# Optimization experiments

Measured on AMD Instinct MI355X. Metric: run time of the kernel, lower is better.

## Reference

```python
import jax, jax.numpy as jnp
import numpy as np

C = 1024
D = C // 8  # query/key channel dim


def setup_inputs() -> dict:
    key = jax.random.key(0)
    ks = jax.random.split(key, 8)
    x = jax.random.normal(ks[0], (8, C, 2048), dtype=jnp.float32)
    # 1x1 Conv1d == per-position linear over channels: weight [out, in], bias [out]
    s_qk = 1.0 / np.sqrt(C)
    Wq = jax.random.uniform(ks[1], (D, C), jnp.float32, -s_qk, s_qk)
    bq = jax.random.uniform(ks[2], (D,), jnp.float32, -s_qk, s_qk)
    Wk = jax.random.uniform(ks[3], (D, C), jnp.float32, -s_qk, s_qk)
    bk = jax.random.uniform(ks[4], (D,), jnp.float32, -s_qk, s_qk)
    Wv = jax.random.uniform(ks[5], (C, C), jnp.float32, -s_qk, s_qk)
    bv = jax.random.uniform(ks[6], (C,), jnp.float32, -s_qk, s_qk)
    gamma = jnp.zeros((1,), dtype=jnp.float32)
    return {"x": x, "Wq": Wq, "bq": bq, "Wk": Wk, "bk": bk, "Wv": Wv, "bv": bv, "gamma": gamma}


def reference(x, Wq, bq, Wk, bk, Wv, bv, gamma):
    # x: [b, c, l]
    q = jnp.einsum('dc,bcl->bdl', Wq, x) + bq[None, :, None]  # [b, d, l]
    k = jnp.einsum('dc,bcl->bdl', Wk, x) + bk[None, :, None]  # [b, d, l]
    v = jnp.einsum('oc,bcl->bol', Wv, x) + bv[None, :, None]  # [b, c, l]
    energy = jnp.einsum('bdi,bdj->bij', q, k)                  # [b, l, l] (no scale, as in source)
    attention = jax.nn.softmax(energy, axis=-1)
    out = jnp.einsum('bcj,bij->bci', v, attention)             # value @ attention^T
    return gamma * out + x
```

## Files before the change

### kernel.cpp

```cpp
#include <hip/hip_runtime.h>
#include <hip/hip_bf16.h>
#include <stdint.h>

#define B_ 8
#define C_ 1024
#define D_ 128
#define L_ 2048

typedef __attribute__((ext_vector_type(8))) short short8;
typedef __attribute__((ext_vector_type(4))) float floatx4;

#define GLDS16(g, l)                                                          \
    __builtin_amdgcn_global_load_lds(                                         \
        (const __attribute__((address_space(1))) uint32_t*)(g),               \
        (__attribute__((address_space(3))) uint32_t*)(l), 16, 0, 0)

__device__ inline float b2f(uint16_t u) {
    union { uint32_t i; float f; } x; x.i = (uint32_t)u << 16; return x.f;
}
__device__ inline uint16_t f2b(float f) {
    union { uint32_t i; float f; } x; x.f = f;
    uint32_t r = (x.i + 0x7fff + ((x.i >> 16) & 1)) >> 16;
    return (uint16_t)r;
}

__global__ void cast_f32_bf16(const float* __restrict__ src, uint16_t* __restrict__ dst, int n) {
    int i = blockIdx.x * 256 + threadIdx.x;
    if (i < n) dst[i] = f2b(src[i]);
}

__global__ __launch_bounds__(256) void transpose_cast(const float* __restrict__ x, uint16_t* __restrict__ xT) {
    __shared__ float tile[32][33];
    int b = blockIdx.z;
    int l0 = blockIdx.x * 32, c0 = blockIdx.y * 32;
    int tx = threadIdx.x, ty = threadIdx.y;
    const float* xb = x + (size_t)b * C_ * L_;
#pragma unroll
    for (int i = 0; i < 4; i++)
        tile[ty + i * 8][tx] = xb[(size_t)(c0 + ty + i * 8) * L_ + l0 + tx];
    __syncthreads();
    uint16_t* xtb = xT + (size_t)b * L_ * C_;
#pragma unroll
    for (int i = 0; i < 4; i++) {
        int l = l0 + ty + i * 8, c = c0 + tx;
        xtb[(size_t)l * C_ + c] = f2b(tile[tx][ty + i * 8]);
    }
}

__global__ __launch_bounds__(256) void gemm_qk(
    const uint16_t* __restrict__ A, const uint16_t* __restrict__ B, long sB,
    const float* __restrict__ bq, const float* __restrict__ bk,
    uint16_t* __restrict__ Cout, long sC, int K) {

    __shared__ uint4 As4[512];
    __shared__ uint4 Bs4[512];
    uint16_t* As = (uint16_t*)As4;
    uint16_t* Bs = (uint16_t*)Bs4;

    const int b = blockIdx.z;
    const uint16_t* Ab = A;
    const uint16_t* Bb = B + (size_t)b * sB;
    const int m0 = blockIdx.y * 128;
    const int n0 = blockIdx.x * 128;

    const int t = threadIdx.x;
    const int lane = t & 63;
    const int wave = t >> 6;
    const int wm = (wave >> 1) * 64;
    const int wn = (wave & 1) * 64;

    floatx4 acc[4][4] = {};

    const int c0 = t, c1 = t + 256;
    const uint16_t* gA0 = Ab + (size_t)(m0 + (c0 >> 2)) * K + (c0 & 3) * 8;
    const uint16_t* gA1 = Ab + (size_t)(m0 + (c1 >> 2)) * K + (c1 & 3) * 8;
    const uint16_t* gB0 = Bb + (size_t)(n0 + (c0 >> 2)) * K + (c0 & 3) * 8;
    const uint16_t* gB1 = Bb + (size_t)(n0 + (c1 >> 2)) * K + (c1 & 3) * 8;

    for (int k0 = 0; k0 < K; k0 += 32) {
        __syncthreads();
        GLDS16(gA0 + k0, &As4[c0]);
        GLDS16(gA1 + k0, &As4[c1]);
        GLDS16(gB0 + k0, &Bs4[c0]);
        GLDS16(gB1 + k0, &Bs4[c1]);
        __syncthreads();

        const int kg = (lane >> 4) * 8;
        const int rA = wm + (lane & 15);
        const int rB = wn + (lane & 15);
        short8 af[4], bf[4];
#pragma unroll
        for (int i = 0; i < 4; i++) af[i] = *(const short8*)(As + (rA + i * 16) * 32 + kg);
#pragma unroll
        for (int j = 0; j < 4; j++) bf[j] = *(const short8*)(Bs + (rB + j * 16) * 32 + kg);
#pragma unroll
        for (int i = 0; i < 4; i++)
#pragma unroll
            for (int j = 0; j < 4; j++)
                acc[i][j] = __builtin_amdgcn_mfma_f32_16x16x32_bf16(af[i], bf[j], acc[i][j], 0, 0, 0);
    }

    uint16_t* Cb = Cout + (size_t)b * sC;
#pragma unroll
    for (int i = 0; i < 4; i++)
#pragma unroll
        for (int j = 0; j < 4; j++) {
            int mrow = m0 + wm + i * 16 + ((lane >> 4) << 2);
            int ncol = n0 + wn + j * 16 + (lane & 15);
#pragma unroll
            for (int r = 0; r < 4; r++) {
                int mr = mrow + r;
                float val = acc[i][j][r] + (mr < 128 ? bq[mr] : bk[mr - 128]);
                Cb[(size_t)ncol * 256 + mr] = f2b(val);
            }
        }
}

template <int EPI>
__global__ __launch_bounds__(512, 2) void gemm256(
    const uint16_t* __restrict__ A, const uint16_t* __restrict__ B,
    int lda, int ldb, long sA, long sB, const float* __restrict__ bias,
    void* __restrict__ Cout, long sC, int ldc, int K,
    const float* __restrict__ gamma, const float* __restrict__ X) {

    __shared__ uint4 As4[2][2048];
    __shared__ uint4 Bs4[2][2048];

    const int b = blockIdx.z;
    const uint16_t* Ab = A + (size_t)b * sA;
    const uint16_t* Bb = B + (size_t)b * sB;
    const int m0 = blockIdx.y * 256;
    const int n0 = blockIdx.x * 256;

    const int t = threadIdx.x;
    const int lane = t & 63;
    const int wid = t >> 6;
    const int wm = (wid >> 2) * 128;
    const int wn = (wid & 3) * 64;

    const int srow = t >> 3;
    const int schunk = (t & 7) * 8;
    const uint16_t* gA = Ab + (size_t)(m0 + srow) * lda + schunk;
    const uint16_t* gB = Bb + (size_t)(n0 + srow) * ldb + schunk;

    floatx4 acc[8][4] = {};
    const int nt = K >> 6;

#define STAGE256(p, k0)                                                      \
    {                                                                        \
        _Pragma("unroll") for (int r = 0; r < 4; r++) {                      \
            GLDS16(gA + (size_t)(64 * r) * lda + (k0), &As4[p][t + 512 * r]);\
            GLDS16(gB + (size_t)(64 * r) * ldb + (k0), &Bs4[p][t + 512 * r]);\
        }                                                                    \
    }

    STAGE256(0, 0);
    __syncthreads();

    for (int kt = 0; kt < nt; kt++) {
        const int cur = kt & 1;
        if (kt + 1 < nt) STAGE256(cur ^ 1, (kt + 1) * 64);

        const uint16_t* Ac = (const uint16_t*)As4[cur];
        const uint16_t* Bc = (const uint16_t*)Bs4[cur];
        const int ra = (wm + (lane & 15)) * 64 + (lane >> 4) * 8;
        const int rb = (wn + (lane & 15)) * 64 + (lane >> 4) * 8;
#pragma unroll
        for (int ks = 0; ks < 2; ks++) {
            short8 af[8], bf[4];
#pragma unroll
            for (int mi = 0; mi < 8; mi++) af[mi] = *(const short8*)(Ac + ra + mi * (16 * 64) + ks * 32);
#pragma unroll
            for (int nj = 0; nj < 4; nj++) bf[nj] = *(const short8*)(Bc + rb + nj * (16 * 64) + ks * 32);
#pragma unroll
            for (int mi = 0; mi < 8; mi++)
#pragma unroll
                for (int nj = 0; nj < 4; nj++)
                    acc[mi][nj] = __builtin_amdgcn_mfma_f32_16x16x32_bf16(af[mi], bf[nj], acc[mi][nj], 0, 0, 0);
        }
        __syncthreads();
    }
#undef STAGE256

    if (EPI == 0 || EPI == 2) {
        uint16_t* Cb = (uint16_t*)Cout + (size_t)b * sC;
#pragma unroll
        for (int mi = 0; mi < 8; mi++)
#pragma unroll
            for (int nj = 0; nj < 4; nj++) {
                int mrow = m0 + wm + mi * 16 + ((lane >> 4) << 2);
                int ncol = n0 + wn + nj * 16 + (lane & 15);
#pragma unroll
                for (int r = 0; r < 4; r++) {
                    float val = acc[mi][nj][r];
                    if (EPI == 0) val += bias[mrow + r];
                    Cb[(size_t)(mrow + r) * ldc + ncol] = f2b(val);
                }
            }
    } else {
        float g = gamma[0];
        float* Ob = (float*)Cout + (size_t)b * sC;
        const float* Xb = X + (size_t)b * sC;
#pragma unroll
        for (int mi = 0; mi < 8; mi++)
#pragma unroll
            for (int nj = 0; nj < 4; nj++) {
                int mrow = m0 + wm + mi * 16 + ((lane >> 4) << 2);
                int ncol = n0 + wn + nj * 16 + (lane & 15);
#pragma unroll
                for (int r = 0; r < 4; r++) {
                    size_t idx = (size_t)(mrow + r) * ldc + ncol;
                    Ob[idx] = g * acc[mi][nj][r] + Xb[idx];
                }
            }
    }
}

__global__ __launch_bounds__(256) void softmax_rows(uint16_t* __restrict__ att) {
    const int i = blockIdx.x, b = blockIdx.y;
    uint16_t* row = att + ((size_t)b * L_ + i) * L_;
    const int t = threadIdx.x;
    short8 v = *(const short8*)(row + t * 8);
    float f[8];
    float m = -1e30f;
#pragma unroll
    for (int e = 0; e < 8; e++) { f[e] = b2f((uint16_t)v[e]); m = fmaxf(m, f[e]); }
#pragma unroll
    for (int off = 32; off >= 1; off >>= 1) m = fmaxf(m, __shfl_xor(m, off));
    __shared__ float redm[4], reds[4];
    const int wave = t >> 6;
    if ((t & 63) == 0) redm[wave] = m;
    __syncthreads();
    m = fmaxf(fmaxf(redm[0], redm[1]), fmaxf(redm[2], redm[3]));
    float s = 0.f;
#pragma unroll
    for (int e = 0; e < 8; e++) { f[e] = __expf(f[e] - m); s += f[e]; }
#pragma unroll
    for (int off = 32; off >= 1; off >>= 1) s += __shfl_xor(s, off);
    if ((t & 63) == 0) reds[wave] = s;
    __syncthreads();
    s = reds[0] + reds[1] + reds[2] + reds[3];
    float inv = 1.0f / s;
    short8 o;
#pragma unroll
    for (int e = 0; e < 8; e++) o[e] = (short)f2b(f[e] * inv);
    *(short8*)(row + t * 8) = o;
}

#define OFF_XT   0ull
#define OFF_QK   33554432ull
#define OFF_V    41943040ull
#define OFF_ATT  75497472ull
#define OFF_WQK  142606336ull
#define OFF_WV   143130624ull

extern "C" void kernel_launch(void* const* d_in, const int* in_sizes, int n_in,
                              void* d_out, int out_size, void* d_ws, size_t ws_size,
                              hipStream_t stream) {
    const float* x  = (const float*)d_in[0];
    const float* Wq = (const float*)d_in[1];
    const float* bq = (const float*)d_in[2];
    const float* Wk = (const float*)d_in[3];
    const float* bk = (const float*)d_in[4];
    const float* Wv = (const float*)d_in[5];
    const float* bv = (const float*)d_in[6];
    const float* gamma = (const float*)d_in[7];
    float* out = (float*)d_out;
    char* ws = (char*)d_ws;

    uint16_t* xT   = (uint16_t*)(ws + OFF_XT);
    uint16_t* qk   = (uint16_t*)(ws + OFF_QK);
    uint16_t* v    = (uint16_t*)(ws + OFF_V);
    uint16_t* att  = (uint16_t*)(ws + OFF_ATT);
    uint16_t* Wqkb = (uint16_t*)(ws + OFF_WQK);
    uint16_t* Wvb  = (uint16_t*)(ws + OFF_WV);

    cast_f32_bf16<<<dim3((D_ * C_ + 255) / 256), 256, 0, stream>>>(Wq, Wqkb, D_ * C_);
    cast_f32_bf16<<<dim3((D_ * C_ + 255) / 256), 256, 0, stream>>>(Wk, Wqkb + D_ * C_, D_ * C_);
    cast_f32_bf16<<<dim3((C_ * C_ + 255) / 256), 256, 0, stream>>>(Wv, Wvb, C_ * C_);

    transpose_cast<<<dim3(L_ / 32, C_ / 32, B_), dim3(32, 8), 0, stream>>>(x, xT);

    gemm_qk<<<dim3(L_ / 128, 2, B_), 256, 0, stream>>>(
        Wqkb, xT, (long)L_ * C_, bq, bk, qk, (long)L_ * 256, C_);

    gemm256<0><<<dim3(L_ / 256, C_ / 256, B_), 512, 0, stream>>>(
        Wvb, xT, C_, C_, 0, (long)L_ * C_, bv, v, (long)C_ * L_, L_, C_, nullptr, nullptr);

    gemm256<2><<<dim3(L_ / 256, L_ / 256, B_), 512, 0, stream>>>(
        qk, qk + 128, 256, 256, (long)L_ * 256, (long)L_ * 256, nullptr,
        att, (long)L_ * L_, L_, D_, nullptr, nullptr);

    softmax_rows<<<dim3(L_, B_), 256, 0, stream>>>(att);

    gemm256<3><<<dim3(L_ / 256, C_ / 256, B_), 512, 0, stream>>>(
        v, att, L_, L_, (long)C_ * L_, (long)L_ * L_, nullptr,
        out, (long)C_ * L_, L_, L_, gamma, x);
}
```

Measured before the change: 355.4 us.

## Restructure gemm256 main loop into 4-stage swizzled LDS pipeline with interleaved MFMA phases

Replaces the double-buffered 64-wide K tile loop with a 4-slot ring of 32-wide K tiles that prefetches three tiles ahead using explicit vmcnt waits. The LDS layout is XOR-swizzled to avoid bank conflicts on the short8 fragment reads. Each iteration is split into two MFMA halves, with the A and B global-to-LDS issues placed between them, and s_setprio raises priority around MFMA bursts. The aim is to hide global load latency and LDS conflicts, at the cost of more barriers per K step and hand-tuned waitcnt logic that is fragile.

```diff
diff --git a/kernel.cpp b/kernel.cpp
--- a/kernel.cpp
+++ b/kernel.cpp
@@ -123,8 +123,8 @@
     void* __restrict__ Cout, long sC, int ldc, int K,
     const float* __restrict__ gamma, const float* __restrict__ X) {
 
-    __shared__ uint4 As4[2][2048];
-    __shared__ uint4 Bs4[2][2048];
+    __shared__ uint4 AS[4][1024];
+    __shared__ uint4 BS[4][1024];
 
     const int b = blockIdx.z;
     const uint16_t* Ab = A + (size_t)b * sA;
@@ -138,49 +138,84 @@
     const int wm = (wid >> 2) * 128;
     const int wn = (wid & 3) * 64;
 
-    const int srow = t >> 3;
-    const int schunk = (t & 7) * 8;
-    const uint16_t* gA = Ab + (size_t)(m0 + srow) * lda + schunk;
-    const uint16_t* gB = Bb + (size_t)(n0 + srow) * ldb + schunk;
+    const int srow = t >> 2;
+    const int sc = ((t & 3) ^ (srow ^ (srow >> 2))) & 3;
+    const uint16_t* gA0 = Ab + (size_t)(m0 + srow) * lda + sc * 8;
+    const uint16_t* gA1 = Ab + (size_t)(m0 + srow + 128) * lda + sc * 8;
+    const uint16_t* gB0 = Bb + (size_t)(n0 + srow) * ldb + sc * 8;
+    const uint16_t* gB1 = Bb + (size_t)(n0 + srow + 128) * ldb + sc * 8;
+
+    const int rsw = ((lane >> 4) ^ (lane ^ (lane >> 2))) & 3;
+    const int aoff = (wm + (lane & 15)) * 32 + rsw * 8;
+    const int boff = (wn + (lane & 15)) * 32 + rsw * 8;
 
     floatx4 acc[8][4] = {};
-    const int nt = K >> 6;
-
-#define STAGE256(p, k0)                                                      \
-    {                                                                        \
-        _Pragma("unroll") for (int r = 0; r < 4; r++) {                      \
-            GLDS16(gA + (size_t)(64 * r) * lda + (k0), &As4[p][t + 512 * r]);\
-            GLDS16(gB + (size_t)(64 * r) * ldb + (k0), &Bs4[p][t + 512 * r]);\
-        }                                                                    \
+    const int nt = K >> 5;
+
+#define STA(slot, k0) do { GLDS16(gA0 + (k0), &AS[slot][t]); GLDS16(gA1 + (k0), &AS[slot][t + 512]); } while (0)
+#define STB(slot, k0) do { GLDS16(gB0 + (k0), &BS[slot][t]); GLDS16(gB1 + (k0), &BS[slot][t + 512]); } while (0)
+
+    STA(0, 0); STB(0, 0);
+    if (nt > 1) { STA(1, 32); STB(1, 32); }
+    if (nt > 2) { STA(2, 64); STB(2, 64); }
+    if (nt > 2)      asm volatile("s_waitcnt vmcnt(8)" ::: "memory");
+    else if (nt > 1) asm volatile("s_waitcnt vmcnt(4)" ::: "memory");
+    else             asm volatile("s_waitcnt vmcnt(0)" ::: "memory");
+    __builtin_amdgcn_s_barrier();
+    __builtin_amdgcn_sched_barrier(0);
+
+    for (int kt = 0; kt < nt; kt++) {
+        const int slot = kt & 3;
+        const uint16_t* Ap = (const uint16_t*)AS[slot];
+        const uint16_t* Bp = (const uint16_t*)BS[slot];
+        const int k3 = (kt + 3) * 32;
+        const bool st = (kt + 3) < nt;
+
+        short8 af[4], bf[4];
+#pragma unroll
+        for (int i = 0; i < 4; i++) af[i] = *(const short8*)(Ap + aoff + i * 512);
+#pragma unroll
+        for (int j = 0; j < 4; j++) bf[j] = *(const short8*)(Bp + boff + j * 512);
+        if (st) STA((kt + 3) & 3, k3);
+        __builtin_amdgcn_s_barrier();
+        asm volatile("s_waitcnt lgkmcnt(0)" ::: "memory");
+        __builtin_amdgcn_sched_barrier(0);
+        __builtin_amdgcn_s_setprio(1);
+#pragma unroll
+        for (int i = 0; i < 4; i++)
+#pragma unroll
+            for (int j = 0; j < 4; j++)
+                acc[i][j] = __builtin_amdgcn_mfma_f32_16x16x32_bf16(af[i], bf[j], acc[i][j], 0, 0, 0);
+        __builtin_amdgcn_s_setprio(0);
+        __builtin_amdgcn_s_barrier();
+        __builtin_amdgcn_sched_barrier(0);
+
+        short8 ag[4];
+#pragma unroll
+        for (int i = 0; i < 4; i++) ag[i] = *(const short8*)(Ap + aoff + (i + 4) * 512);
+        if (st) STB((kt + 3) & 3, k3);
+        __builtin_amdgcn_s_barrier();
+        asm volatile("s_waitcnt lgkmcnt(0)" ::: "memory");
+        __builtin_amdgcn_sched_barrier(0);
+        __builtin_amdgcn_s_setprio(1);
+#pragma unroll
+        for (int i = 0; i < 4; i++)
+#pragma unroll
+            for (int j = 0; j < 4; j++)
+                acc[i + 4][j] = __builtin_amdgcn_mfma_f32_16x16x32_bf16(ag[i], bf[j], acc[i + 4][j], 0, 0, 0);
+        __builtin_amdgcn_s_setprio(0);
+
+        if (kt + 1 < nt) {
+            const int ahead = nt - 2 - kt;
+            if (ahead >= 2)      asm volatile("s_waitcnt vmcnt(8)" ::: "memory");
+            else if (ahead == 1) asm volatile("s_waitcnt vmcnt(4)" ::: "memory");
+            else                 asm volatile("s_waitcnt vmcnt(0)" ::: "memory");
+            __builtin_amdgcn_s_barrier();
+            __builtin_amdgcn_sched_barrier(0);
+        }
     }
-
-    STAGE256(0, 0);
-    __syncthreads();
-
-    for (int kt = 0; kt < nt; kt++) {
-        const int cur = kt & 1;
-        if (kt + 1 < nt) STAGE256(cur ^ 1, (kt + 1) * 64);
-
-        const uint16_t* Ac = (const uint16_t*)As4[cur];
-        const uint16_t* Bc = (const uint16_t*)Bs4[cur];
-        const int ra = (wm + (lane & 15)) * 64 + (lane >> 4) * 8;
-        const int rb = (wn + (lane & 15)) * 64 + (lane >> 4) * 8;
-#pragma unroll
-        for (int ks = 0; ks < 2; ks++) {
-            short8 af[8], bf[4];
-#pragma unroll
-            for (int mi = 0; mi < 8; mi++) af[mi] = *(const short8*)(Ac + ra + mi * (16 * 64) + ks * 32);
-#pragma unroll
-            for (int nj = 0; nj < 4; nj++) bf[nj] = *(const short8*)(Bc + rb + nj * (16 * 64) + ks * 32);
-#pragma unroll
-            for (int mi = 0; mi < 8; mi++)
-#pragma unroll
-                for (int nj = 0; nj < 4; nj++)
-                    acc[mi][nj] = __builtin_amdgcn_mfma_f32_16x16x32_bf16(af[mi], bf[nj], acc[mi][nj], 0, 0, 0);
-        }
-        __syncthreads();
-    }
-#undef STAGE256
+#undef STA
+#undef STB
 
     if (EPI == 0 || EPI == 2) {
         uint16_t* Cb = (uint16_t*)Cout + (size_t)b * sC;
```

New measurement: 341.8 us. 3.8% less time.
